# Performance work log

Measured on AMD Instinct MI355X. Metric: run time of the kernel, lower is better.

Reference implementation:

```python
import jax, jax.numpy as jnp
import numpy as np

B, N_CLS, M_TIME, U_LAB = 1024, 96, 256, 40


def setup_inputs() -> dict:
    key = jax.random.key(0)
    k1, k2, k3 = jax.random.split(key, 3)
    logits = jax.random.normal(k1, (B, N_CLS, M_TIME), dtype=jnp.float32)
    # module treats inputs as per-timestep class probabilities (softmax output of CRNN)
    out_padded = jax.nn.softmax(logits, axis=1)
    label = jax.random.randint(k2, (B, U_LAB), 1, N_CLS, dtype=jnp.int32)  # 0 is blank
    unpadded_w = jax.random.randint(k3, (B,), 512, 4 * M_TIME + 1, dtype=jnp.int32)
    return {"out_padded": out_padded, "label": label, "unpadded_w": unpadded_w}


def _alpha(probs, lab, T, L):
    # probs: (M, N) time-major class probabilities; lab: (U,) label indices; T traced int.
    # Faithful to compute_alpha: per-timestep renormalization over [start, end),
    # recurrence computed for s in [start, L).
    M = probs.shape[0]
    s_idx = jnp.arange(L)
    i_idx = jnp.maximum((s_idx - 1) // 2, 0)
    is_odd = (s_idx % 2) == 1
    cls = jnp.where(is_odd, lab[i_idx], 0)  # blank = class 0 for even s
    # skip (a[t-1][s-2]) allowed only for odd s != 1 with non-repeated label
    skip = is_odd & (s_idx != 1) & (lab[i_idx] != lab[jnp.maximum(i_idx - 1, 0)])

    p0 = probs[0]
    row0 = jnp.zeros((L,), probs.dtype).at[0].set(p0[0]).at[1].set(p0[lab[0]])
    c0 = row0[0] + row0[1]
    row0 = jnp.where((s_idx < 2) & (c0 > 0), row0 / jnp.where(c0 > 0, c0, 1.0), row0)

    def step(prev, t):
        start = jnp.maximum(0, L - 2 * (T - t))
        end = jnp.minimum(2 * t + 2, L)
        pm1 = jnp.concatenate([jnp.zeros((1,), prev.dtype), prev[:-1]])
        pm2 = jnp.concatenate([jnp.zeros((2,), prev.dtype), prev[:-2]])
        val = (prev
               + jnp.where(s_idx > 0, pm1, 0.0)
               + jnp.where(skip, pm2, 0.0)) * probs[t, cls]
        val = jnp.where(s_idx >= start, val, 0.0)  # s < start stays zero
        nmask = (s_idx >= start) & (s_idx < end)
        c = jnp.sum(jnp.where(nmask, val, 0.0))
        val = jnp.where(nmask & (c > 0), val / jnp.where(c > 0, c, 1.0), val)
        return val, val

    _, rows = jax.lax.scan(step, row0, jnp.arange(1, M))
    a = jnp.concatenate([row0[None, :], rows], axis=0)  # (M, L)
    return jnp.where((jnp.arange(M) < T)[:, None], a, 0.0)  # rows >= T are zero


def _ctc_single(out_cw, lab, w):
    probs = out_cw.T  # (M, N): time x classes, as in torch.transpose(out, 1, 0)
    M = probs.shape[0]
    U = lab.shape[0]
    L = 2 * U + 1
    T = w // 4
    a = _alpha(probs, lab, T, L)
    # 'beta' faithful to source: alpha on CLASS-flipped probs (torch.fliplr on (T,N))
    # with reversed labels, then flipud+fliplr of the (T,L) result.
    b_raw = _alpha(probs[:, ::-1], lab[::-1], T, L)
    src = T - 1 - jnp.arange(M)
    valid = (src >= 0) & (src < M)
    b = jnp.where(valid[:, None], b_raw[jnp.clip(src, 0, M - 1)], 0.0)[:, ::-1]
    ab = a * b  # (M, L)
    s_idx = jnp.arange(L)
    cls = jnp.where((s_idx % 2) == 1, lab[jnp.maximum((s_idx - 1) // 2, 0)], 0)
    lh = jnp.sum(ab / probs[:, cls], axis=1)  # (M,)
    tmask = jnp.arange(M) < T
    return -jnp.sum(jnp.where(tmask, jnp.log(jnp.where(tmask, lh, 1.0)), 0.0))


def reference(out_padded, label, unpadded_w):
    losses = jax.vmap(_ctc_single)(out_padded, label, unpadded_w)  # (B,)
    return jnp.sum(losses)
```

## Files before the change

### kernel.cpp

```cpp
#include <hip/hip_runtime.h>
#include <cmath>

namespace {
constexpr int BN = 1024;
constexpr int NC = 96;
constexpr int MT = 256;
constexpr int UL = 40;
constexpr int LS = 81;
constexpr int PAIRS = 41;

template <int CTRL>
__device__ __forceinline__ float dppf(float v) {
  return __builtin_bit_cast(
      float, __builtin_amdgcn_update_dpp(0, __builtin_bit_cast(int, v), CTRL,
                                         0xf, 0xf, true));
}
__device__ __forceinline__ float rl63(float x) {
  return __builtin_bit_cast(
      float, __builtin_amdgcn_readlane(__builtin_bit_cast(int, x), 63));
}
__device__ __forceinline__ float wave_sum(float x) {
  x += dppf<0x111>(x);
  x += dppf<0x112>(x);
  x += dppf<0x114>(x);
  x += dppf<0x118>(x);
  x += dppf<0x142>(x);
  x += dppf<0x143>(x);
  return rl63(x);
}
__device__ __forceinline__ float wave_shr1(float v) { return dppf<0x138>(v); }
__device__ __forceinline__ float fast_rcp(float x) {
  return __builtin_amdgcn_rcpf(x);
}
__device__ __forceinline__ unsigned packu(float a, float b) {
  unsigned ua = __builtin_bit_cast(unsigned, a) >> 16;
  unsigned ub = __builtin_bit_cast(unsigned, b) & 0xffff0000u;
  return ua | ub;
}
__device__ __forceinline__ float bf_lo(unsigned u) {
  return __builtin_bit_cast(float, u << 16);
}
__device__ __forceinline__ float bf_hi(unsigned u) {
  return __builtin_bit_cast(float, u & 0xffff0000u);
}

constexpr float FQ = 1e8f;
constexpr float SEPS = 1e-30f;
constexpr float GB = 1099511627776.0f;

__global__ __launch_bounds__(64) void chain_kernel(
    const float* __restrict__ gout, const int* __restrict__ glabel,
    const int* __restrict__ gw, unsigned* __restrict__ xa,
    unsigned* __restrict__ xb) {
  const int bx = blockIdx.x;
  const int b = bx >> 1, ph = bx & 1;
  const int i = threadIdx.x;
  const float* P = gout + (size_t)b * (NC * MT);
  const int* lab = glabel + b * UL;
  const int T = gw[b] >> 2;

  const int s0 = 2 * i, s1 = s0 + 1;
  const float h0f = (i <= 40) ? 1.f : 0.f;
  const float h1f = (i <= 39) ? 1.f : 0.f;
  const int iw = (i <= 40) ? i : 40;
  const bool act = (i <= 40);

  const float* pB;
  const float* pL;
  float mskf;
  unsigned* outp;
  if (ph == 0) {
    const int li = (i < UL) ? lab[i] : 0;
    const int lm = (i >= 1 && i < UL) ? lab[i - 1] : 0;
    pB = P;
    pL = P + (size_t)li * MT;
    mskf = (i >= 1 && i <= 39 && li != lm) ? 1.f : 0.f;
    outp = xa + (size_t)b * MT * PAIRS + iw;
  } else {
    const int rli = (i < UL) ? lab[UL - 1 - i] : 0;
    const int rlm = (i >= 1 && i < UL) ? lab[UL - i] : 0;
    pB = P + (size_t)(NC - 1) * MT;
    pL = P + (size_t)(NC - 1 - rli) * MT;
    mskf = (i >= 1 && i <= 39 && rli != rlm) ? 1.f : 0.f;
    outp = xb + (size_t)b * MT * PAIRS + (40 - iw);
  }

  float pbv[16], plv[16];
  float4 LA = *(const float4*)(pB + 0),  LB = *(const float4*)(pB + 4);
  float4 LC = *(const float4*)(pB + 8),  LD = *(const float4*)(pB + 12);
  float4 MA = *(const float4*)(pL + 0),  MB = *(const float4*)(pL + 4);
  float4 MC = *(const float4*)(pL + 8),  MD = *(const float4*)(pL + 12);
  pbv[0] = LA.x;  pbv[1] = LA.y;  pbv[2] = LA.z;  pbv[3] = LA.w;
  pbv[4] = LB.x;  pbv[5] = LB.y;  pbv[6] = LB.z;  pbv[7] = LB.w;
  pbv[8] = LC.x;  pbv[9] = LC.y;  pbv[10] = LC.z; pbv[11] = LC.w;
  pbv[12] = LD.x; pbv[13] = LD.y; pbv[14] = LD.z; pbv[15] = LD.w;
  plv[0] = MA.x;  plv[1] = MA.y;  plv[2] = MA.z;  plv[3] = MA.w;
  plv[4] = MB.x;  plv[5] = MB.y;  plv[6] = MB.z;  plv[7] = MB.w;
  plv[8] = MC.x;  plv[9] = MC.y;  plv[10] = MC.z; plv[11] = MC.w;
  plv[12] = MD.x; plv[13] = MD.y; plv[14] = MD.z; plv[15] = MD.w;
  LA = *(const float4*)(pB + 16); LB = *(const float4*)(pB + 20);
  LC = *(const float4*)(pB + 24); LD = *(const float4*)(pB + 28);
  MA = *(const float4*)(pL + 16); MB = *(const float4*)(pL + 20);
  MC = *(const float4*)(pL + 24); MD = *(const float4*)(pL + 28);

  float v0 = (i == 0) ? pbv[0] : 0.f;
  float v1 = (i == 0) ? plv[0] : 0.f;

  float f0[16], f1[16], sv[16];
  if (ph == 0) {
    sv[0] = v0 + v1;
    f0[0] = (i == 0) ? 1.f : 0.f;
    f1[0] = f0[0];
    v0 *= FQ;
    v1 *= FQ;
  } else {
    v0 *= FQ;
    v1 *= FQ;
    sv[0] = v0 + v1;
    f0[0] = v0;
    f1[0] = 0.f;
  }

#define CTC_STEP(T_, K_, DOMASK, BOOST)                               \
  {                                                                   \
    float pm1 = wave_shr1(v1);                                        \
    if (ph == 1 && (K_) >= 1) f1[(K_)-1] = pm1;                       \
    if (BOOST) { v0 *= GB; v1 *= GB; pm1 *= GB; }                     \
    float u0 = v0 + pm1;                                              \
    float u1 = (v0 + v1) + pm1 * mskf;                                \
    if (DOMASK) {                                                     \
      const int start_ = LS - 2 * (T - (T_));                         \
      if (s0 < start_) u0 = 0.f;                                      \
      if (s1 < start_) u1 = 0.f;                                      \
    }                                                                 \
    const float x0 = u0 * h0f, x1 = u1 * h1f;                         \
    float n0 = x0 * pbv[(K_)];                                        \
    float n1 = x1 * plv[(K_)];                                        \
    sv[(K_)] = n0 + n1;                                               \
    v0 = n0; v1 = n1;                                                 \
    if (ph == 0) { f0[(K_)] = x0; f1[(K_)] = x1; }                    \
    else { f0[(K_)] = n0; }                                           \
  }

#define WS_LEVEL(CTRL)                                                \
  {                                                                   \
    _Pragma("unroll")                                                 \
    for (int k = 0; k < 16; ++k) sv[k] += dppf<CTRL>(sv[k]);          \
  }

#define CTC_BURST(T0_)                                                \
  {                                                                   \
    if (ph == 1) f1[15] = wave_shr1(v1);         \
    WS_LEVEL(0x111) WS_LEVEL(0x112) WS_LEVEL(0x114)                   \
    WS_LEVEL(0x118) WS_LEVEL(0x142) WS_LEVEL(0x143)                   \
    _Pragma("unroll")                                                 \
    for (int k = 0; k < 16; ++k) sv[k] = rl63(sv[k]);                 \
    if (act) {                                                        \
      unsigned ob[16];                                                \
      _Pragma("unroll")                                               \
      for (int k = 0; k < 16; ++k) {                                  \
        float inv = fast_rcp(fmaxf(sv[k], SEPS));                     \
        ob[k] = packu(f0[k] * inv, f1[k] * inv);                      \
      }                                                               \
      if ((T0_) + 15 < T) {                                           \
        _Pragma("unroll")                                             \
        for (int k = 0; k < 16; ++k)                                  \
          outp[((T0_) + k) * PAIRS] = ob[k];      \
      } else {                                                        \
        _Pragma("unroll")                                             \
        for (int k = 0; k < 16; ++k)                                  \
          if ((T0_) + k < T) outp[((T0_) + k) * PAIRS] = ob[k];       \
      }                                                               \
    }                                                                 \
    float rb = FQ * fast_rcp(fmaxf(sv[15], SEPS));                    \
    rb = fminf(fmaxf(rb, 1e-20f), 1e20f);                             \
    v0 *= rb; v1 *= rb;                                               \
  }

#define CTC_UNPACK(T0_)                                               \
  {                                                                   \
    pbv[0] = LA.x;  pbv[1] = LA.y;  pbv[2] = LA.z;  pbv[3] = LA.w;    \
    pbv[4] = LB.x;  pbv[5] = LB.y;  pbv[6] = LB.z;  pbv[7] = LB.w;    \
    pbv[8] = LC.x;  pbv[9] = LC.y;  pbv[10] = LC.z; pbv[11] = LC.w;   \
    pbv[12] = LD.x; pbv[13] = LD.y; pbv[14] = LD.z; pbv[15] = LD.w;   \
    plv[0] = MA.x;  plv[1] = MA.y;  plv[2] = MA.z;  plv[3] = MA.w;    \
    plv[4] = MB.x;  plv[5] = MB.y;  plv[6] = MB.z;  plv[7] = MB.w;    \
    plv[8] = MC.x;  plv[9] = MC.y;  plv[10] = MC.z; plv[11] = MC.w;   \
    plv[12] = MD.x; plv[13] = MD.y; plv[14] = MD.z; plv[15] = MD.w;   \
    int np = (T0_) + 16;                                              \
    if (np > 240) np = 240;                                           \
    LA = *(const float4*)(pB + np);      LB = *(const float4*)(pB + np + 4);  \
    LC = *(const float4*)(pB + np + 8);  LD = *(const float4*)(pB + np + 12); \
    MA = *(const float4*)(pL + np);      MB = *(const float4*)(pL + np + 4);  \
    MC = *(const float4*)(pL + np + 8);  MD = *(const float4*)(pL + np + 12); \
  }

#pragma unroll
  for (int k = 1; k < 8; ++k) CTC_STEP(k, k, false, 0);
  CTC_STEP(8, 8, false, 1);
#pragma unroll
  for (int k = 9; k < 16; ++k) CTC_STEP(k, k, false, 0);
  CTC_BURST(0);

  int t0 = 16;
  for (; t0 + 56 <= T; t0 += 16) {
    CTC_UNPACK(t0);
#pragma unroll
    for (int k = 0; k < 8; ++k) CTC_STEP(t0 + k, k, false, 0);
    CTC_STEP(t0 + 8, 8, false, 1);
#pragma unroll
    for (int k = 9; k < 16; ++k) CTC_STEP(t0 + k, k, false, 0);
    CTC_BURST(t0);
  }
  for (; t0 < T; t0 += 16) {
    CTC_UNPACK(t0);
#pragma unroll
    for (int k = 0; k < 8; ++k) CTC_STEP(t0 + k, k, true, 0);
    CTC_STEP(t0 + 8, 8, true, 1);
#pragma unroll
    for (int k = 9; k < 16; ++k) CTC_STEP(t0 + k, k, true, 0);
    CTC_BURST(t0);
  }
#undef CTC_STEP
#undef CTC_BURST
#undef CTC_UNPACK
#undef WS_LEVEL
}

__global__ __launch_bounds__(256) void combine_kernel(
    const int* __restrict__ gw, const unsigned* __restrict__ xa,
    const unsigned* __restrict__ xb, float* __restrict__ loss_out) {
  const int b = blockIdx.x;
  const int tid = threadIdx.x;
  const int T = gw[b] >> 2;
  float lsum = 0.f;
  if (tid < T) {
    const unsigned* A = xa + ((size_t)b * MT + tid) * PAIRS;
    const unsigned* Bb = xb + ((size_t)b * MT + (T - 1 - tid)) * PAIRS;
    float d = 0.f;
#pragma unroll
    for (int p = 0; p < PAIRS; ++p) {
      const unsigned av = A[p];
      const unsigned bv = Bb[p];
      d = fmaf(bf_lo(av), bf_lo(bv), d);
      d = fmaf(bf_hi(av), bf_hi(bv), d);
    }
    lsum = -__logf(fmaxf(d, 1e-37f));
  }
  lsum = wave_sum(lsum);
  __shared__ float part[4];
  if ((tid & 63) == 0) part[tid >> 6] = lsum;
  __syncthreads();
  if (tid == 0) {
    float L = part[0] + part[1] + part[2] + part[3];
    loss_out[b] = fminf(fmaxf(L, -1e30f), 1e30f);
  }
}

__global__ void reduce_kernel(const float* __restrict__ loss_in,
                              float* __restrict__ out) {
  __shared__ double sm[256];
  const int tid = threadIdx.x;
  double s = 0.0;
  for (int k = tid; k < BN; k += 256) s += (double)loss_in[k];
  sm[tid] = s;
  __syncthreads();
  for (int w = 128; w >= 1; w >>= 1) {
    if (tid < w) sm[tid] += sm[tid + w];
    __syncthreads();
  }
  if (tid == 0) out[0] = (float)sm[0];
}
}

extern "C" void kernel_launch(void* const* d_in, const int* in_sizes, int n_in,
                              void* d_out, int out_size, void* d_ws, size_t ws_size,
                              hipStream_t stream) {
  const float* gout = (const float*)d_in[0];
  const int* glabel = (const int*)d_in[1];
  const int* gw = (const int*)d_in[2];
  unsigned* xa = (unsigned*)d_ws;
  unsigned* xb = xa + (size_t)BN * MT * PAIRS;
  float* loss = (float*)(xb + (size_t)BN * MT * PAIRS);
  chain_kernel<<<2 * BN, 64, 0, stream>>>(gout, glabel, gw, xa, xb);
  combine_kernel<<<BN, 256, 0, stream>>>(gw, xa, xb, loss);
  reduce_kernel<<<1, 256, 0, stream>>>(loss, (float*)d_out);
}
```

Measured before the change: 183.9 us.

## Stream unnormalized alpha/beta pairs per step and defer normalization to combine

The chain kernel no longer buffers 16 steps of f0/f1 values in registers for normalization at each burst. Instead it writes the raw packed bf16 pair at every step and stores the per-timestep wave sums to new sa/sb workspace arrays. The combine kernel then loads these sums and applies the reciprocals while forming the dot product. The aim is to cut register pressure and the per-burst store spike in the serial chain. The cost is extra sum traffic, extra multiplies in combine, and packing unnormalized values to bf16, which relies on the wide bf16 exponent range.

```diff
diff --git a/kernel.cpp b/kernel.cpp
--- a/kernel.cpp
+++ b/kernel.cpp
@@ -51,7 +51,8 @@
 __global__ __launch_bounds__(64) void chain_kernel(
     const float* __restrict__ gout, const int* __restrict__ glabel,
     const int* __restrict__ gw, unsigned* __restrict__ xa,
-    unsigned* __restrict__ xb) {
+    unsigned* __restrict__ xb, float* __restrict__ sa,
+    float* __restrict__ sb) {
   const int bx = blockIdx.x;
   const int b = bx >> 1, ph = bx & 1;
   const int i = threadIdx.x;
@@ -69,6 +70,7 @@
   const float* pL;
   float mskf;
   unsigned* outp;
+  float* sump;
   if (ph == 0) {
     const int li = (i < UL) ? lab[i] : 0;
     const int lm = (i >= 1 && i < UL) ? lab[i - 1] : 0;
@@ -76,6 +78,7 @@
     pL = P + (size_t)li * MT;
     mskf = (i >= 1 && i <= 39 && li != lm) ? 1.f : 0.f;
     outp = xa + (size_t)b * MT * PAIRS + iw;
+    sump = sa + (size_t)b * MT;
   } else {
     const int rli = (i < UL) ? lab[UL - 1 - i] : 0;
     const int rlm = (i >= 1 && i < UL) ? lab[UL - i] : 0;
@@ -83,6 +86,7 @@
     pL = P + (size_t)(NC - 1 - rli) * MT;
     mskf = (i >= 1 && i <= 39 && rli != rlm) ? 1.f : 0.f;
     outp = xb + (size_t)b * MT * PAIRS + (40 - iw);
+    sump = sb + (size_t)b * MT;
   }
 
   float pbv[16], plv[16];
@@ -106,25 +110,30 @@
   float v0 = (i == 0) ? pbv[0] : 0.f;
   float v1 = (i == 0) ? plv[0] : 0.f;
 
-  float f0[16], f1[16], sv[16];
+  float sv[16];
+  float prev_n0 = 0.f;
   if (ph == 0) {
     sv[0] = v0 + v1;
-    f0[0] = (i == 0) ? 1.f : 0.f;
-    f1[0] = f0[0];
+    if (act) {
+      const float f00 = (i == 0) ? 1.f : 0.f;
+      outp[0] = packu(f00, f00);
+    }
     v0 *= FQ;
     v1 *= FQ;
   } else {
     v0 *= FQ;
     v1 *= FQ;
     sv[0] = v0 + v1;
-    f0[0] = v0;
-    f1[0] = 0.f;
-  }
-
-#define CTC_STEP(T_, K_, DOMASK, BOOST)                               \
+    prev_n0 = v0;
+  }
+
+#define CTC_STEP(T_, K_, DOMASK, BOOST, GUARD)                        \
   {                                                                   \
     float pm1 = wave_shr1(v1);                                        \
-    if (ph == 1 && (K_) >= 1) f1[(K_)-1] = pm1;                       \
+    if (ph == 1 && (K_) >= 1) {                                       \
+      if (act && (!(GUARD) || ((T_)-1) < T))                          \
+        outp[((T_)-1) * PAIRS] = packu(prev_n0, pm1);                 \
+    }                                                                 \
     if (BOOST) { v0 *= GB; v1 *= GB; pm1 *= GB; }                     \
     float u0 = v0 + pm1;                                              \
     float u1 = (v0 + v1) + pm1 * mskf;                                \
@@ -137,9 +146,11 @@
     float n0 = x0 * pbv[(K_)];                                        \
     float n1 = x1 * plv[(K_)];                                        \
     sv[(K_)] = n0 + n1;                                               \
-    v0 = n0; v1 = n1;                                                 \
-    if (ph == 0) { f0[(K_)] = x0; f1[(K_)] = x1; }                    \
-    else { f0[(K_)] = n0; }                                           \
+    if (ph == 0) {                                                    \
+      if (act && (!(GUARD) || (T_) < T))                              \
+        outp[(T_) * PAIRS] = packu(x0, x1);                           \
+    }                                                                 \
+    v0 = n0; v1 = n1; prev_n0 = n0;                                   \
   }
 
 #define WS_LEVEL(CTRL)                                                \
@@ -148,30 +159,22 @@
     for (int k = 0; k < 16; ++k) sv[k] += dppf<CTRL>(sv[k]);          \
   }
 
-#define CTC_BURST(T0_)                                                \
-  {                                                                   \
-    if (ph == 1) f1[15] = wave_shr1(v1);         \
+#define CTC_BURST(T0_, GUARD)                                         \
+  {                                                                   \
+    if (ph == 1) {                                                    \
+      float fl = wave_shr1(v1);                                       \
+      if (act && (!(GUARD) || ((T0_) + 15) < T))                      \
+        outp[((T0_) + 15) * PAIRS] = packu(prev_n0, fl);              \
+    }                                                                 \
     WS_LEVEL(0x111) WS_LEVEL(0x112) WS_LEVEL(0x114)                   \
     WS_LEVEL(0x118) WS_LEVEL(0x142) WS_LEVEL(0x143)                   \
     _Pragma("unroll")                                                 \
     for (int k = 0; k < 16; ++k) sv[k] = rl63(sv[k]);                 \
-    if (act) {                                                        \
-      unsigned ob[16];                                                \
-      _Pragma("unroll")                                               \
-      for (int k = 0; k < 16; ++k) {                                  \
-        float inv = fast_rcp(fmaxf(sv[k], SEPS));                     \
-        ob[k] = packu(f0[k] * inv, f1[k] * inv);                      \
-      }                                                               \
-      if ((T0_) + 15 < T) {                                           \
-        _Pragma("unroll")                                             \
-        for (int k = 0; k < 16; ++k)                                  \
-          outp[((T0_) + k) * PAIRS] = ob[k];      \
-      } else {                                                        \
-        _Pragma("unroll")                                             \
-        for (int k = 0; k < 16; ++k)                                  \
-          if ((T0_) + k < T) outp[((T0_) + k) * PAIRS] = ob[k];       \
-      }                                                               \
-    }                                                                 \
+    float ssel = sv[0];                                               \
+    _Pragma("unroll")                                                 \
+    for (int k = 1; k < 16; ++k) ssel = (i == k) ? sv[k] : ssel;      \
+    if (i < 16 && (!(GUARD) || ((T0_) + i) < T))                      \
+      sump[(T0_) + i] = ssel;                                         \
     float rb = FQ * fast_rcp(fmaxf(sv[15], SEPS));                    \
     rb = fminf(fmaxf(rb, 1e-20f), 1e20f);                             \
     v0 *= rb; v1 *= rb;                                               \
@@ -196,30 +199,30 @@
   }
 
 #pragma unroll
-  for (int k = 1; k < 8; ++k) CTC_STEP(k, k, false, 0);
-  CTC_STEP(8, 8, false, 1);
-#pragma unroll
-  for (int k = 9; k < 16; ++k) CTC_STEP(k, k, false, 0);
-  CTC_BURST(0);
+  for (int k = 1; k < 8; ++k) CTC_STEP(k, k, false, 0, 0);
+  CTC_STEP(8, 8, false, 1, 0);
+#pragma unroll
+  for (int k = 9; k < 16; ++k) CTC_STEP(k, k, false, 0, 0);
+  CTC_BURST(0, 0);
 
   int t0 = 16;
   for (; t0 + 56 <= T; t0 += 16) {
     CTC_UNPACK(t0);
 #pragma unroll
-    for (int k = 0; k < 8; ++k) CTC_STEP(t0 + k, k, false, 0);
-    CTC_STEP(t0 + 8, 8, false, 1);
-#pragma unroll
-    for (int k = 9; k < 16; ++k) CTC_STEP(t0 + k, k, false, 0);
-    CTC_BURST(t0);
+    for (int k = 0; k < 8; ++k) CTC_STEP(t0 + k, k, false, k == 8 ? 1 : 0, 0);
+    CTC_STEP(t0 + 8, 8, false, 1, 0);
+#pragma unroll
+    for (int k = 9; k < 16; ++k) CTC_STEP(t0 + k, k, false, 0, 0);
+    CTC_BURST(t0, 0);
   }
   for (; t0 < T; t0 += 16) {
     CTC_UNPACK(t0);
 #pragma unroll
-    for (int k = 0; k < 8; ++k) CTC_STEP(t0 + k, k, true, 0);
-    CTC_STEP(t0 + 8, 8, true, 1);
-#pragma unroll
-    for (int k = 9; k < 16; ++k) CTC_STEP(t0 + k, k, true, 0);
-    CTC_BURST(t0);
+    for (int k = 0; k < 8; ++k) CTC_STEP(t0 + k, k, true, 0, 1);
+    CTC_STEP(t0 + 8, 8, true, 1, 1);
+#pragma unroll
+    for (int k = 9; k < 16; ++k) CTC_STEP(t0 + k, k, true, 0, 1);
+    CTC_BURST(t0, 1);
   }
 #undef CTC_STEP
 #undef CTC_BURST
@@ -229,7 +232,8 @@
 
 __global__ __launch_bounds__(256) void combine_kernel(
     const int* __restrict__ gw, const unsigned* __restrict__ xa,
-    const unsigned* __restrict__ xb, float* __restrict__ loss_out) {
+    const unsigned* __restrict__ xb, const float* __restrict__ sa,
+    const float* __restrict__ sb, float* __restrict__ loss_out) {
   const int b = blockIdx.x;
   const int tid = threadIdx.x;
   const int T = gw[b] >> 2;
@@ -237,13 +241,16 @@
   if (tid < T) {
     const unsigned* A = xa + ((size_t)b * MT + tid) * PAIRS;
     const unsigned* Bb = xb + ((size_t)b * MT + (T - 1 - tid)) * PAIRS;
+    const float invA = fast_rcp(fmaxf(sa[(size_t)b * MT + tid], SEPS));
+    const float invB =
+        fast_rcp(fmaxf(sb[(size_t)b * MT + (T - 1 - tid)], SEPS));
     float d = 0.f;
 #pragma unroll
     for (int p = 0; p < PAIRS; ++p) {
       const unsigned av = A[p];
       const unsigned bv = Bb[p];
-      d = fmaf(bf_lo(av), bf_lo(bv), d);
-      d = fmaf(bf_hi(av), bf_hi(bv), d);
+      d = fmaf(bf_lo(av) * invA, bf_lo(bv) * invB, d);
+      d = fmaf(bf_hi(av) * invA, bf_hi(bv) * invB, d);
     }
     lsum = -__logf(fmaxf(d, 1e-37f));
   }
@@ -281,8 +288,10 @@
   const int* gw = (const int*)d_in[2];
   unsigned* xa = (unsigned*)d_ws;
   unsigned* xb = xa + (size_t)BN * MT * PAIRS;
-  float* loss = (float*)(xb + (size_t)BN * MT * PAIRS);
-  chain_kernel<<<2 * BN, 64, 0, stream>>>(gout, glabel, gw, xa, xb);
-  combine_kernel<<<BN, 256, 0, stream>>>(gw, xa, xb, loss);
+  float* sa = (float*)(xb + (size_t)BN * MT * PAIRS);
+  float* sb = sa + (size_t)BN * MT;
+  float* loss = sb + (size_t)BN * MT;
+  chain_kernel<<<2 * BN, 64, 0, stream>>>(gout, glabel, gw, xa, xb, sa, sb);
+  combine_kernel<<<BN, 256, 0, stream>>>(gw, xa, xb, sa, sb, loss);
   reduce_kernel<<<1, 256, 0, stream>>>(loss, (float*)d_out);
 }
```

Measured after the change: 190.4 us. 3.5% more time.

## Defer per-block normalization burst to overlap with next recurrence round

Applied to the files above, without the earlier changes.

The 16-step block recurrence is double-buffered into A/B register sets. The end of each round now computes only the single wave reduction it needs for renormalizing the carried state. The full 16-way reduction, reciprocal and output stores for the previous block are deferred and interleaved with the next block's serial recurrence, hiding the DPP reduction latency behind the dependent chain. This doubles the per-step buffers, which raises register pressure and adds a redundant reduction of the last step.

```diff
diff --git a/kernel.cpp b/kernel.cpp
--- a/kernel.cpp
+++ b/kernel.cpp
@@ -106,25 +106,26 @@
   float v0 = (i == 0) ? pbv[0] : 0.f;
   float v1 = (i == 0) ? plv[0] : 0.f;
 
-  float f0[16], f1[16], sv[16];
+  float f0A[16], f1A[16], svA[16];
+  float f0B[16], f1B[16], svB[16];
   if (ph == 0) {
-    sv[0] = v0 + v1;
-    f0[0] = (i == 0) ? 1.f : 0.f;
-    f1[0] = f0[0];
+    svA[0] = v0 + v1;
+    f0A[0] = (i == 0) ? 1.f : 0.f;
+    f1A[0] = f0A[0];
     v0 *= FQ;
     v1 *= FQ;
   } else {
     v0 *= FQ;
     v1 *= FQ;
-    sv[0] = v0 + v1;
-    f0[0] = v0;
-    f1[0] = 0.f;
-  }
-
-#define CTC_STEP(T_, K_, DOMASK, BOOST)                               \
+    svA[0] = v0 + v1;
+    f0A[0] = v0;
+    f1A[0] = 0.f;
+  }
+
+#define CTC_STEP(S, T_, K_, DOMASK, BOOST)                            \
   {                                                                   \
     float pm1 = wave_shr1(v1);                                        \
-    if (ph == 1 && (K_) >= 1) f1[(K_)-1] = pm1;                       \
+    if (ph == 1 && (K_) >= 1) f1##S[(K_)-1] = pm1;                    \
     if (BOOST) { v0 *= GB; v1 *= GB; pm1 *= GB; }                     \
     float u0 = v0 + pm1;                                              \
     float u1 = (v0 + v1) + pm1 * mskf;                                \
@@ -136,43 +137,68 @@
     const float x0 = u0 * h0f, x1 = u1 * h1f;                         \
     float n0 = x0 * pbv[(K_)];                                        \
     float n1 = x1 * plv[(K_)];                                        \
-    sv[(K_)] = n0 + n1;                                               \
+    sv##S[(K_)] = n0 + n1;                                            \
     v0 = n0; v1 = n1;                                                 \
-    if (ph == 0) { f0[(K_)] = x0; f1[(K_)] = x1; }                    \
-    else { f0[(K_)] = n0; }                                           \
-  }
-
-#define WS_LEVEL(CTRL)                                                \
-  {                                                                   \
-    _Pragma("unroll")                                                 \
-    for (int k = 0; k < 16; ++k) sv[k] += dppf<CTRL>(sv[k]);          \
-  }
-
-#define CTC_BURST(T0_)                                                \
-  {                                                                   \
-    if (ph == 1) f1[15] = wave_shr1(v1);         \
-    WS_LEVEL(0x111) WS_LEVEL(0x112) WS_LEVEL(0x114)                   \
-    WS_LEVEL(0x118) WS_LEVEL(0x142) WS_LEVEL(0x143)                   \
-    _Pragma("unroll")                                                 \
-    for (int k = 0; k < 16; ++k) sv[k] = rl63(sv[k]);                 \
+    if (ph == 0) { f0##S[(K_)] = x0; f1##S[(K_)] = x1; }              \
+    else { f0##S[(K_)] = n0; }                                        \
+  }
+
+#define CTC_ROUNDEND(S)                                               \
+  {                                                                   \
+    if (ph == 1) f1##S[15] = wave_shr1(v1);                           \
+    float w_ = sv##S[15];                                             \
+    w_ += dppf<0x111>(w_); w_ += dppf<0x112>(w_);                     \
+    w_ += dppf<0x114>(w_); w_ += dppf<0x118>(w_);                     \
+    w_ += dppf<0x142>(w_); w_ += dppf<0x143>(w_);                     \
+    float rb = FQ * fast_rcp(fmaxf(rl63(w_), SEPS));                  \
+    rb = fminf(fmaxf(rb, 1e-20f), 1e20f);                             \
+    v0 *= rb; v1 *= rb;                                               \
+  }
+
+#define WS_LEVEL(S, CTRL)                                             \
+  {                                                                   \
+    _Pragma("unroll")                                                 \
+    for (int k = 0; k < 16; ++k) sv##S[k] += dppf<CTRL>(sv##S[k]);    \
+  }
+
+#define CTC_DEFBURST(S, T0_)                                          \
+  {                                                                   \
+    WS_LEVEL(S, 0x111) WS_LEVEL(S, 0x112) WS_LEVEL(S, 0x114)          \
+    WS_LEVEL(S, 0x118) WS_LEVEL(S, 0x142) WS_LEVEL(S, 0x143)          \
+    _Pragma("unroll")                                                 \
+    for (int k = 0; k < 16; ++k) sv##S[k] = rl63(sv##S[k]);           \
     if (act) {                                                        \
       unsigned ob[16];                                                \
       _Pragma("unroll")                                               \
       for (int k = 0; k < 16; ++k) {                                  \
-        float inv = fast_rcp(fmaxf(sv[k], SEPS));                     \
-        ob[k] = packu(f0[k] * inv, f1[k] * inv);                      \
+        float inv = fast_rcp(fmaxf(sv##S[k], SEPS));                  \
+        ob[k] = packu(f0##S[k] * inv, f1##S[k] * inv);                \
       }                                                               \
-      if ((T0_) + 15 < T) {                                           \
-        _Pragma("unroll")                                             \
-        for (int k = 0; k < 16; ++k)                                  \
-          outp[((T0_) + k) * PAIRS] = ob[k];      \
-      } else {                                                        \
-        _Pragma("unroll")                                             \
-        for (int k = 0; k < 16; ++k)                                  \
-          if ((T0_) + k < T) outp[((T0_) + k) * PAIRS] = ob[k];       \
+      _Pragma("unroll")                                               \
+      for (int k = 0; k < 16; ++k)                                    \
+        outp[((T0_) + k) * PAIRS] = ob[k];        \
+    }                                                                 \
+  }
+
+#define CTC_TAILBURST(S, T0_)                                         \
+  {                                                                   \
+    if (ph == 1) f1##S[15] = wave_shr1(v1);      \
+    WS_LEVEL(S, 0x111) WS_LEVEL(S, 0x112) WS_LEVEL(S, 0x114)          \
+    WS_LEVEL(S, 0x118) WS_LEVEL(S, 0x142) WS_LEVEL(S, 0x143)          \
+    _Pragma("unroll")                                                 \
+    for (int k = 0; k < 16; ++k) sv##S[k] = rl63(sv##S[k]);           \
+    if (act) {                                                        \
+      unsigned ob[16];                                                \
+      _Pragma("unroll")                                               \
+      for (int k = 0; k < 16; ++k) {                                  \
+        float inv = fast_rcp(fmaxf(sv##S[k], SEPS));                  \
+        ob[k] = packu(f0##S[k] * inv, f1##S[k] * inv);                \
       }                                                               \
+      _Pragma("unroll")                                               \
+      for (int k = 0; k < 16; ++k)                                    \
+        if ((T0_) + k < T) outp[((T0_) + k) * PAIRS] = ob[k];         \
     }                                                                 \
-    float rb = FQ * fast_rcp(fmaxf(sv[15], SEPS));                    \
+    float rb = FQ * fast_rcp(fmaxf(sv##S[15], SEPS));                 \
     rb = fminf(fmaxf(rb, 1e-20f), 1e20f);                             \
     v0 *= rb; v1 *= rb;                                               \
   }
@@ -195,35 +221,54 @@
     MC = *(const float4*)(pL + np + 8);  MD = *(const float4*)(pL + np + 12); \
   }
 
-#pragma unroll
-  for (int k = 1; k < 8; ++k) CTC_STEP(k, k, false, 0);
-  CTC_STEP(8, 8, false, 1);
-#pragma unroll
-  for (int k = 9; k < 16; ++k) CTC_STEP(k, k, false, 0);
-  CTC_BURST(0);
+#define CTC_ROUND(S, T0_)                                             \
+  {                                                                   \
+    CTC_UNPACK(T0_);                                                  \
+    _Pragma("unroll")                                                 \
+    for (int k = 0; k < 8; ++k) CTC_STEP(S, (T0_) + k, k, false, 0);  \
+    CTC_STEP(S, (T0_) + 8, 8, false, 1);                              \
+    _Pragma("unroll")                                                 \
+    for (int k = 9; k < 16; ++k) CTC_STEP(S, (T0_) + k, k, false, 0); \
+    CTC_ROUNDEND(S);                                                  \
+  }
+
+#pragma unroll
+  for (int k = 1; k < 8; ++k) CTC_STEP(A, k, k, false, 0);
+  CTC_STEP(A, 8, 8, false, 1);
+#pragma unroll
+  for (int k = 9; k < 16; ++k) CTC_STEP(A, k, k, false, 0);
+  CTC_ROUNDEND(A);
 
   int t0 = 16;
-  for (; t0 + 56 <= T; t0 += 16) {
-    CTC_UNPACK(t0);
-#pragma unroll
-    for (int k = 0; k < 8; ++k) CTC_STEP(t0 + k, k, false, 0);
-    CTC_STEP(t0 + 8, 8, false, 1);
-#pragma unroll
-    for (int k = 9; k < 16; ++k) CTC_STEP(t0 + k, k, false, 0);
-    CTC_BURST(t0);
+  for (; t0 + 72 <= T; t0 += 32) {
+    CTC_ROUND(B, t0);
+    CTC_DEFBURST(A, t0 - 16);
+    CTC_ROUND(A, t0 + 16);
+    CTC_DEFBURST(B, t0);
+  }
+  if (t0 + 56 <= T) {
+    CTC_ROUND(B, t0);
+    CTC_DEFBURST(A, t0 - 16);
+    CTC_DEFBURST(B, t0);
+    t0 += 16;
+  } else {
+    CTC_DEFBURST(A, t0 - 16);
   }
   for (; t0 < T; t0 += 16) {
     CTC_UNPACK(t0);
 #pragma unroll
-    for (int k = 0; k < 8; ++k) CTC_STEP(t0 + k, k, true, 0);
-    CTC_STEP(t0 + 8, 8, true, 1);
-#pragma unroll
-    for (int k = 9; k < 16; ++k) CTC_STEP(t0 + k, k, true, 0);
-    CTC_BURST(t0);
+    for (int k = 0; k < 8; ++k) CTC_STEP(A, t0 + k, k, true, 0);
+    CTC_STEP(A, t0 + 8, 8, true, 1);
+#pragma unroll
+    for (int k = 9; k < 16; ++k) CTC_STEP(A, t0 + k, k, true, 0);
+    CTC_TAILBURST(A, t0);
   }
 #undef CTC_STEP
-#undef CTC_BURST
+#undef CTC_ROUNDEND
+#undef CTC_DEFBURST
+#undef CTC_TAILBURST
 #undef CTC_UNPACK
+#undef CTC_ROUND
 #undef WS_LEVEL
 }
 
```

After: 184.6 us. Within noise of the previous version (+0.4%).
